# Performance work log

Hardware: AMD Instinct MI355X
Metric: run time of the kernel (lower is better)

The kernel has to match this reference:

```python
import jax, jax.numpy as jnp
import numpy as np

E = 1024
H = 16
HD = 64
DI = E // 16  # 64, GRU hidden size
VOCAB = 32000
B, T = 2, 2048


def adaptive_pool_matrix(l_in, l_out):
    # PyTorch AdaptiveAvgPool1d: out[i] = mean(in[floor(i*l_in/l_out) : ceil((i+1)*l_in/l_out)])
    P = np.zeros((l_in, l_out), np.float32)
    for i in range(l_out):
        s = (i * l_in) // l_out
        e = -((-(i + 1) * l_in) // l_out)
        P[s:e, i] = 1.0 / (e - s)
    return jnp.asarray(P)


def gru(x, wih, whh):
    # x: [B, T, DI]; wih/whh: [3*DI, DI]; no bias; gate order (r, z, n)
    h_dim = whh.shape[1]
    xw = jnp.einsum('btd,gd->btg', x, wih)  # [B, T, 3*DI]

    def step(h, xw_t):
        hw = h @ whh.T
        r = jax.nn.sigmoid(xw_t[:, :h_dim] + hw[:, :h_dim])
        z = jax.nn.sigmoid(xw_t[:, h_dim:2 * h_dim] + hw[:, h_dim:2 * h_dim])
        n = jnp.tanh(xw_t[:, 2 * h_dim:] + r * hw[:, 2 * h_dim:])
        h_new = (1.0 - z) * n + z * h
        return h_new, h_new

    h0 = jnp.zeros((x.shape[0], h_dim), x.dtype)
    _, hs = jax.lax.scan(step, h0, jnp.swapaxes(xw, 0, 1))
    return jnp.swapaxes(hs, 0, 1)  # [B, T, DI]


def pos_embed(x, gru_wih, gru_whh, lin_w, p_pos, p_proj):
    # x: [B, T, E]. Pools act on the feature dim (torch last-dim after permute).
    x_proj = x @ p_proj            # [B, T, E-DI]
    pos = gru(x @ p_pos, gru_wih, gru_whh)  # [B, T, DI]
    out = jnp.concatenate([pos, x_proj], axis=-1) @ lin_w.T
    return out + x


def layernorm(x, w, b, eps=1e-5):
    mu = jnp.mean(x, axis=-1, keepdims=True)
    var = jnp.var(x, axis=-1, keepdims=True)
    return (x - mu) * jax.lax.rsqrt(var + eps) * w + b


def setup_inputs() -> dict:
    key = jax.random.key(0)
    ks = jax.random.split(key, 16)
    s = 0.02
    return {
        'x': jax.random.normal(ks[0], (B, T, E), jnp.float32),
        'token_ids': jax.random.randint(ks[1], (B, T), 0, VOCAB, jnp.int32),
        'q_gru_wih': jax.random.normal(ks[2], (3 * DI, DI), jnp.float32) * s,
        'q_gru_whh': jax.random.normal(ks[3], (3 * DI, DI), jnp.float32) * s,
        'q_lin_w': jax.random.normal(ks[4], (E, E), jnp.float32) * s,
        'k_gru_wih': jax.random.normal(ks[5], (3 * DI, DI), jnp.float32) * s,
        'k_gru_whh': jax.random.normal(ks[6], (3 * DI, DI), jnp.float32) * s,
        'k_lin_w': jax.random.normal(ks[7], (E, E), jnp.float32) * s,
        'v_emb': jax.random.normal(ks[8], (VOCAB, E), jnp.float32) * s + 1.0,
        'q_ln_w': jnp.ones((E,), jnp.float32),
        'q_ln_b': jnp.zeros((E,), jnp.float32),
        'k_ln_w': jnp.ones((E,), jnp.float32),
        'k_ln_b': jnp.zeros((E,), jnp.float32),
        'out_w': jax.random.normal(ks[9], (E, E), jnp.float32) * s,
        'out_b': jnp.zeros((E,), jnp.float32),
    }


def reference(x, token_ids, q_gru_wih, q_gru_whh, q_lin_w, k_gru_wih, k_gru_whh,
              k_lin_w, v_emb, q_ln_w, q_ln_b, k_ln_w, k_ln_b, out_w, out_b):
    p_pos = adaptive_pool_matrix(E, DI)
    p_proj = adaptive_pool_matrix(E, E - DI)

    q = pos_embed(x, q_gru_wih, q_gru_whh, q_lin_w, p_pos, p_proj)
    k = pos_embed(x, k_gru_wih, k_gru_whh, k_lin_w, p_pos, p_proj)
    v = jax.nn.silu(x) * v_emb[token_ids]  # [B, T, E]

    q = layernorm(q, q_ln_w, q_ln_b)
    k = layernorm(k, k_ln_w, k_ln_b)

    # [B, T, E] -> [B, H, T, HD]
    def split_heads(t):
        return t.reshape(B, T, H, HD).transpose(0, 2, 1, 3)

    qh, kh, vh = split_heads(q), split_heads(k), split_heads(v)

    scores = jnp.einsum('bhtd,bhsd->bhts', qh, kh) / jnp.sqrt(jnp.float32(HD))
    # Original code: attn_weights += attn_weights.masked_fill(mask, -inf)
    # => unmasked scores are DOUBLED; masked (future) positions become -inf.
    causal = jnp.triu(jnp.ones((T, T), bool), k=1)  # True above diagonal
    scores = jnp.where(causal, -jnp.inf, scores * 2.0)
    attn = jax.nn.softmax(scores, axis=-1)

    out = jnp.einsum('bhts,bhsd->bhtd', attn, vh)  # [B, H, T, HD]
    out = out.transpose(0, 2, 1, 3).reshape(B, T, E)
    return out @ out_w.T + out_b
```

## Files before the change

kernel.cpp:

```cpp
#include <hip/hip_runtime.h>


namespace {

constexpr int B_ = 2, T_ = 2048, E_ = 1024, H_ = 16, HD_ = 64, G3_ = 192, M_ = B_ * T_;
constexpr float SRg = -1.4426950408889634f;
constexpr float SNg = 2.8853900817779268f;

typedef _Float16 f16;
typedef _Float16 f16x8 __attribute__((ext_vector_type(8)));
typedef _Float16 f16x4 __attribute__((ext_vector_type(4)));
typedef _Float16 f16x2 __attribute__((ext_vector_type(2)));
typedef float f32x4 __attribute__((ext_vector_type(4)));

__device__ __forceinline__ f32x4 mfma16(f16x8 a, f16x8 b, f32x4 c) {
  return __builtin_amdgcn_mfma_f32_16x16x32_f16(a, b, c, 0, 0, 0);
}

#if __has_builtin(__builtin_amdgcn_fdot2)
__device__ __forceinline__ float fdot2(f16x2 a, f16x2 b, float c) {
  return __builtin_amdgcn_fdot2(a, b, c, false);
}
#else
__device__ __forceinline__ float fdot2(f16x2 a, f16x2 b, float c) {
  return c + (float)a[0] * (float)b[0] + (float)a[1] * (float)b[1];
}
#endif

__device__ __forceinline__ float exp2_(float x) {
#if __has_builtin(__builtin_amdgcn_exp2f)
  return __builtin_amdgcn_exp2f(x);
#else
  return exp2f(x);
#endif
}
__device__ __forceinline__ float rcp_(float x) {
#if __has_builtin(__builtin_amdgcn_rcpf)
  return __builtin_amdgcn_rcpf(x);
#else
  return 1.f / x;
#endif
}

__global__ __launch_bounds__(256) void k_cvt(const float* __restrict__ s,
                                             f16* __restrict__ d, int n) {
  int i = (blockIdx.x * 256 + threadIdx.x) * 4;
  if (i < n) {
    float4 v = *(const float4*)(s + i);
    f16x4 o = {(f16)v.x, (f16)v.y, (f16)v.z, (f16)v.w};
    *(f16x4*)(d + i) = o;
  }
}

__global__ __launch_bounds__(256) void k_prep(
    const float* __restrict__ x, const int* __restrict__ tok,
    const f16* __restrict__ wihq, const f16* __restrict__ wihk,
    const float* __restrict__ v_emb,
    f16* __restrict__ vh, f16* __restrict__ aq, f16* __restrict__ ak,
    float* __restrict__ xwq, float* __restrict__ xwk) {
  __shared__ float xs[E_];
  __shared__ float xp[64];
  const int row = blockIdx.x;
  const int b = row >> 11, t = row & (T_ - 1);
  const int tid = threadIdx.x;
  const float* xrow = x + (size_t)row * E_;
  {
    const int tk = tok[row];
    float4 xv = ((const float4*)xrow)[tid];
    ((float4*)xs)[tid] = xv;
    float4 ev = ((const float4*)(v_emb + (size_t)tk * E_))[tid];
    f16x4 o;
    o[0] = (f16)(xv.x / (1.f + __expf(-xv.x)) * ev.x);
    o[1] = (f16)(xv.y / (1.f + __expf(-xv.y)) * ev.y);
    o[2] = (f16)(xv.z / (1.f + __expf(-xv.z)) * ev.z);
    o[3] = (f16)(xv.w / (1.f + __expf(-xv.w)) * ev.w);
    const int e0 = tid * 4;
    const size_t voff = ((size_t)(b * H_ + (e0 >> 6)) * T_ + t) * HD_ + (e0 & 63);
    *(f16x4*)(vh + voff) = o;
  }
  __syncthreads();
  if (tid < 64) {
    float s = 0.f;
#pragma unroll
    for (int j = 0; j < 16; ++j) s += xs[tid * 16 + j];
    xp[tid] = s * (1.f / 16.f);
  }
  for (int i = tid; i < 960; i += 256) {
    int s0 = (i * 1024) / 960;
    int e0 = ((i + 1) * 1024 + 959) / 960;
    float m = xs[s0];
    if (e0 - s0 == 2) m = (m + xs[s0 + 1]) * 0.5f;
    f16 hv = (f16)m;
    aq[(size_t)row * E_ + 64 + i] = hv;
    ak[(size_t)row * E_ + 64 + i] = hv;
  }
  __syncthreads();
  for (int o = tid; o < 2 * G3_; o += 256) {
    const int chain = o / G3_, g = o % G3_;
    const f16* wrow = (chain ? wihk : wihq) + g * 64;
    float acc = 0.f;
#pragma unroll
    for (int c = 0; c < 8; ++c) {
      f16x8 wv = *(const f16x8*)(wrow + c * 8);
#pragma unroll
      for (int u = 0; u < 8; ++u) acc += xp[c * 8 + u] * (float)wv[u];
    }
    const float sc = (g < 128) ? SRg : SNg;
    (chain ? xwk : xwq)[(size_t)row * G3_ + g] = acc * sc;
  }
}

__device__ __forceinline__ void gru_core(const float* __restrict__ xw,
                                         const float* __restrict__ whh,
                                         f16* __restrict__ a, int lane) {
  f16x2 wr[32], wz[32], wn[32];
#pragma unroll
  for (int i = 0; i < 32; ++i) {
    wr[i] = {(f16)(whh[(size_t)lane * 64 + i] * SRg),
             (f16)(whh[(size_t)lane * 64 + i + 32] * SRg)};
    wz[i] = {(f16)(whh[(size_t)(64 + lane) * 64 + i] * SRg),
             (f16)(whh[(size_t)(64 + lane) * 64 + i + 32] * SRg)};
    wn[i] = {(f16)(whh[(size_t)(128 + lane) * 64 + i] * SNg),
             (f16)(whh[(size_t)(128 + lane) * 64 + i + 32] * SNg)};
  }
  float h = 0.f;
  float xr = xw[lane], xz = xw[64 + lane], xn = xw[128 + lane];
  for (int t = 0; t < T_; ++t) {
    const unsigned hu = (unsigned)__builtin_bit_cast(unsigned short, (f16)h);
    int va = (int)hu, vb = (int)hu;
    asm volatile("v_permlane32_swap_b32 %0, %1" : "+v"(va), "+v"(vb));
    const int pk = (int)(hu | ((unsigned)va << 16));
    int hp[32];
#pragma unroll
    for (int i = 0; i < 32; ++i) hp[i] = __builtin_amdgcn_readlane(pk, i);
    const int tn = (t + 1 < T_) ? t + 1 : t;
    const float* nx = xw + (size_t)tn * G3_;
    const float nxr = nx[lane], nxz = nx[64 + lane], nxn = nx[128 + lane];
    float ar = xr;
#pragma unroll
    for (int i = 0; i < 32; ++i)
      ar = fdot2(wr[i], __builtin_bit_cast(f16x2, hp[i]), ar);
    const float r = rcp_(1.f + exp2_(ar));
    float an = 0.f;
#pragma unroll
    for (int i = 0; i < 32; ++i)
      an = fdot2(wn[i], __builtin_bit_cast(f16x2, hp[i]), an);
    const float p2 = fmaf(r, an, xn);
    const float n = fmaf(-2.f, rcp_(1.f + exp2_(p2)), 1.f);
    float az = xz;
#pragma unroll
    for (int i = 0; i < 32; ++i)
      az = fdot2(wz[i], __builtin_bit_cast(f16x2, hp[i]), az);
    const float z = rcp_(1.f + exp2_(az));
    h = fmaf(z, h - n, n);
    a[(size_t)t * E_ + lane] = (f16)h;
    xr = nxr; xz = nxz; xn = nxn;
  }
}

__global__ __launch_bounds__(256, 1) void k_mega(
    const float* __restrict__ xwq, const float* __restrict__ xwk,
    const float* __restrict__ whhq, const float* __restrict__ whhk,
    f16* __restrict__ aq, f16* __restrict__ ak,
    const f16* __restrict__ WQ, const f16* __restrict__ WK,
    float* __restrict__ QPRE, float* __restrict__ KPRE,
    const float* __restrict__ out_w, f16* __restrict__ WO) {
  __shared__ __align__(16) f16 As[128][72];
  __shared__ __align__(16) f16 Bs[128][72];
  const int bx = blockIdx.x;
  const int tid = threadIdx.x;
  if (bx == 0) {
    const int wid = tid >> 6, lane = tid & 63;
    const int qk = wid >> 1, b = wid & 1;
    const float* xw = (qk ? xwk : xwq) + (size_t)b * T_ * G3_;
    const float* whh = qk ? whhk : whhq;
    f16* a = (qk ? ak : aq) + (size_t)b * T_ * E_;
    gru_core(xw, whh, a, lane);
    return;
  }
  if (bx <= 512) {
    const int bid = bx - 1;
    const int chain = bid >> 8, tile = bid & 255;
    const int m0 = (tile >> 3) * 128, n0 = (tile & 7) * 128;
    const f16* A = chain ? ak : aq;
    const f16* W = chain ? WK : WQ;
    float* C = chain ? KPRE : QPRE;
    const int wid = tid >> 6, lane = tid & 63;
    const int wr = wid >> 1, wc = wid & 1;
    const int lg = lane >> 4, lc = lane & 15;
    f32x4 acc[4][4] = {};
    for (int kt = 64; kt < E_; kt += 64) {
#pragma unroll
      for (int it = 0; it < 4; ++it) {
        const int r = it * 32 + (tid >> 3);
        const int cs = (tid & 7) * 8;
        *(f16x8*)&As[r][cs] = *(const f16x8*)(A + (size_t)(m0 + r) * E_ + kt + cs);
        *(f16x8*)&Bs[r][cs] = *(const f16x8*)(W + (size_t)(n0 + r) * E_ + kt + cs);
      }
      __syncthreads();
      f16x8 af[4][2], bf[4][2];
#pragma unroll
      for (int mi = 0; mi < 4; ++mi)
#pragma unroll
        for (int ks = 0; ks < 2; ++ks) {
          af[mi][ks] = *(const f16x8*)&As[wr * 64 + mi * 16 + lc][ks * 32 + lg * 8];
          bf[mi][ks] = *(const f16x8*)&Bs[wc * 64 + mi * 16 + lc][ks * 32 + lg * 8];
        }
#pragma unroll
      for (int mi = 0; mi < 4; ++mi)
#pragma unroll
        for (int ni = 0; ni < 4; ++ni)
#pragma unroll
          for (int ks = 0; ks < 2; ++ks)
            acc[mi][ni] = mfma16(af[mi][ks], bf[ni][ks], acc[mi][ni]);
      __syncthreads();
    }
#pragma unroll
    for (int mi = 0; mi < 4; ++mi) {
      const int r0 = m0 + wr * 64 + mi * 16 + lg * 4;
#pragma unroll
      for (int ni = 0; ni < 4; ++ni) {
        const int col = n0 + wc * 64 + ni * 16 + lc;
#pragma unroll
        for (int q = 0; q < 4; ++q)
          C[(size_t)(r0 + q) * E_ + col] = acc[mi][ni][q];
      }
    }
    return;
  }
  {
    const int cb = bx - 513;
    for (int i = cb * 256 + tid; i < E_ * E_ / 4; i += 8 * 256) {
      float4 v = ((const float4*)out_w)[i];
      f16x4 o = {(f16)v.x, (f16)v.y, (f16)v.z, (f16)v.w};
      *(f16x4*)(WO + (size_t)i * 4) = o;
    }
  }
}

__global__ __launch_bounds__(256) void k_fix(
    const f16* __restrict__ aq, const f16* __restrict__ ak,
    const f16* __restrict__ WQ, const f16* __restrict__ WK,
    const float* __restrict__ x, float* __restrict__ QPRE,
    float* __restrict__ KPRE) {
  __shared__ __align__(16) f16 As[128][72];
  __shared__ __align__(16) f16 Bs[128][72];
  const int chain = blockIdx.z;
  const f16* A = chain ? ak : aq;
  const f16* W = chain ? WK : WQ;
  float* C = chain ? KPRE : QPRE;
  const int m0 = blockIdx.x * 128, n0 = blockIdx.y * 128;
  const int tid = threadIdx.x;
  const int wid = tid >> 6, lane = tid & 63;
  const int wr = wid >> 1, wc = wid & 1;
  const int lg = lane >> 4, lc = lane & 15;
#pragma unroll
  for (int it = 0; it < 4; ++it) {
    const int r = it * 32 + (tid >> 3);
    const int cs = (tid & 7) * 8;
    *(f16x8*)&As[r][cs] = *(const f16x8*)(A + (size_t)(m0 + r) * E_ + cs);
    *(f16x8*)&Bs[r][cs] = *(const f16x8*)(W + (size_t)(n0 + r) * E_ + cs);
  }
  __syncthreads();
  f32x4 acc[4][4] = {};
  f16x8 af[4][2], bf[4][2];
#pragma unroll
  for (int mi = 0; mi < 4; ++mi)
#pragma unroll
    for (int ks = 0; ks < 2; ++ks) {
      af[mi][ks] = *(const f16x8*)&As[wr * 64 + mi * 16 + lc][ks * 32 + lg * 8];
      bf[mi][ks] = *(const f16x8*)&Bs[wc * 64 + mi * 16 + lc][ks * 32 + lg * 8];
    }
#pragma unroll
  for (int mi = 0; mi < 4; ++mi)
#pragma unroll
    for (int ni = 0; ni < 4; ++ni)
#pragma unroll
      for (int ks = 0; ks < 2; ++ks)
        acc[mi][ni] = mfma16(af[mi][ks], bf[ni][ks], acc[mi][ni]);
#pragma unroll
  for (int mi = 0; mi < 4; ++mi) {
    const int r0 = m0 + wr * 64 + mi * 16 + lg * 4;
#pragma unroll
    for (int ni = 0; ni < 4; ++ni) {
      const int col = n0 + wc * 64 + ni * 16 + lc;
#pragma unroll
      for (int q = 0; q < 4; ++q) {
        const size_t idx = (size_t)(r0 + q) * E_ + col;
        C[idx] += acc[mi][ni][q] + x[idx];
      }
    }
  }
}

__global__ __launch_bounds__(256) void k_ln(
    const float* __restrict__ qpre, const float* __restrict__ kpre,
    const float* __restrict__ qw, const float* __restrict__ qb,
    const float* __restrict__ kw, const float* __restrict__ kb,
    f16* __restrict__ qh, f16* __restrict__ kh) {
  const int chain = blockIdx.y;
  const float* pre = chain ? kpre : qpre;
  const float* gw = chain ? kw : qw;
  const float* gb = chain ? kb : qb;
  f16* outp = chain ? kh : qh;
  const int row = blockIdx.x;
  const int tid = threadIdx.x;
  const float4 v = ((const float4*)(pre + (size_t)row * E_))[tid];
  float s = v.x + v.y + v.z + v.w;
  float s2 = v.x * v.x + v.y * v.y + v.z * v.z + v.w * v.w;
#pragma unroll
  for (int off = 32; off; off >>= 1) {
    s += __shfl_xor(s, off);
    s2 += __shfl_xor(s2, off);
  }
  __shared__ float red[8];
  const int wid = tid >> 6, lane = tid & 63;
  if (!lane) { red[wid] = s; red[4 + wid] = s2; }
  __syncthreads();
  s = red[0] + red[1] + red[2] + red[3];
  s2 = red[4] + red[5] + red[6] + red[7];
  const float mu = s * (1.f / E_);
  const float inv = rsqrtf(s2 * (1.f / E_) - mu * mu + 1e-5f);
  const float4 w4 = ((const float4*)gw)[tid];
  const float4 b4 = ((const float4*)gb)[tid];
  const int e0 = tid * 4;
  f16x4 o;
  o[0] = (f16)((v.x - mu) * inv * w4.x + b4.x);
  o[1] = (f16)((v.y - mu) * inv * w4.y + b4.y);
  o[2] = (f16)((v.z - mu) * inv * w4.z + b4.z);
  o[3] = (f16)((v.w - mu) * inv * w4.w + b4.w);
  const int b = row >> 11, t = row & (T_ - 1);
  const size_t off2 = ((size_t)(b * H_ + (e0 >> 6)) * T_ + t) * HD_ + (e0 & 63);
  *(f16x4*)(outp + off2) = o;
}

__global__ __launch_bounds__(256) void k_attn(const f16* __restrict__ Q,
                                              const f16* __restrict__ K,
                                              const f16* __restrict__ V,
                                              f16* __restrict__ AO) {
  __shared__ __align__(16) f16 Kt[64][72];
  __shared__ __align__(16) f16 Vt[64][72];
  __shared__ __align__(16) f16 Ps[4][16][72];
  const int qi = blockIdx.x, bh = blockIdx.y;
  const int b = bh >> 4, h = bh & 15;
  const int tid = threadIdx.x, wid = tid >> 6, lane = tid & 63;
  const int lg = lane >> 4, lc = lane & 15;
  const size_t hbase = (size_t)bh * T_ * HD_;
  const int qb = qi * 64;
  f16x8 qf[2];
  {
    const int qrow = qb + wid * 16 + lc;
#pragma unroll
    for (int ks = 0; ks < 2; ++ks)
      qf[ks] = *(const f16x8*)(Q + hbase + (size_t)qrow * HD_ + ks * 32 + lg * 8);
  }
  f32x4 o[4] = {};
  float m_run[4] = {-1e30f, -1e30f, -1e30f, -1e30f};
  float l_run[4] = {};
  const int qrow_d = qb + wid * 16 + lg * 4;
  for (int kt = 0; kt <= qi; ++kt) {
    {
      const int r = tid >> 2, cs = (tid & 3) * 16;
      const f16* ksrc = K + hbase + (size_t)(kt * 64 + r) * HD_ + cs;
      *(f16x8*)&Kt[r][cs] = *(const f16x8*)ksrc;
      *(f16x8*)&Kt[r][cs + 8] = *(const f16x8*)(ksrc + 8);
      const f16* vsrc = V + hbase + (size_t)(kt * 64 + lane) * HD_ + wid * 16;
      f16x8 va = *(const f16x8*)vsrc;
      f16x8 vb = *(const f16x8*)(vsrc + 8);
#pragma unroll
      for (int u = 0; u < 8; ++u) {
        Vt[wid * 16 + u][lane] = va[u];
        Vt[wid * 16 + 8 + u][lane] = vb[u];
      }
    }
    __syncthreads();
    f32x4 s[4] = {};
#pragma unroll
    for (int nt = 0; nt < 4; ++nt)
#pragma unroll
      for (int ks = 0; ks < 2; ++ks) {
        f16x8 kf = *(const f16x8*)&Kt[nt * 16 + lc][ks * 32 + lg * 8];
        s[nt] = mfma16(qf[ks], kf, s[nt]);
      }
    const bool diag = (kt == qi);
#pragma unroll
    for (int nt = 0; nt < 4; ++nt) {
      const int colg = kt * 64 + nt * 16 + lc;
#pragma unroll
      for (int r = 0; r < 4; ++r) {
        float v = s[nt][r] * 0.25f;
        if (diag && colg > qrow_d + r) v = -1e30f;
        s[nt][r] = v;
      }
    }
    float scalev[4];
#pragma unroll
    for (int r = 0; r < 4; ++r) {
      float m = fmaxf(fmaxf(s[0][r], s[1][r]), fmaxf(s[2][r], s[3][r]));
#pragma unroll
      for (int of = 1; of < 16; of <<= 1) m = fmaxf(m, __shfl_xor(m, of));
      const float mn = fmaxf(m_run[r], m);
      scalev[r] = __expf(m_run[r] - mn);
      m_run[r] = mn;
    }
    float ladd[4] = {};
#pragma unroll
    for (int nt = 0; nt < 4; ++nt)
#pragma unroll
      for (int r = 0; r < 4; ++r) {
        const float p = __expf(s[nt][r] - m_run[r]);
        s[nt][r] = p;
        ladd[r] += p;
      }
#pragma unroll
    for (int r = 0; r < 4; ++r) {
      float la = ladd[r];
#pragma unroll
      for (int of = 1; of < 16; of <<= 1) la += __shfl_xor(la, of);
      l_run[r] = l_run[r] * scalev[r] + la;
      o[0][r] *= scalev[r];
      o[1][r] *= scalev[r];
      o[2][r] *= scalev[r];
      o[3][r] *= scalev[r];
    }
#pragma unroll
    for (int nt = 0; nt < 4; ++nt)
#pragma unroll
      for (int r = 0; r < 4; ++r)
        Ps[wid][lg * 4 + r][nt * 16 + lc] = (f16)s[nt][r];
    f16x8 pf[2];
#pragma unroll
    for (int ks = 0; ks < 2; ++ks)
      pf[ks] = *(const f16x8*)&Ps[wid][lc][ks * 32 + lg * 8];
#pragma unroll
    for (int nt = 0; nt < 4; ++nt)
#pragma unroll
      for (int ks = 0; ks < 2; ++ks) {
        f16x8 vf = *(const f16x8*)&Vt[nt * 16 + lc][ks * 32 + lg * 8];
        o[nt] = mfma16(pf[ks], vf, o[nt]);
      }
    __syncthreads();
  }
#pragma unroll
  for (int nt = 0; nt < 4; ++nt)
#pragma unroll
    for (int r = 0; r < 4; ++r) {
      const float val = o[nt][r] / l_run[r];
      const int qrow = qrow_d + r;
      AO[((size_t)(b * T_ + qrow)) * E_ + h * HD_ + nt * 16 + lc] = (f16)val;
    }
}

__global__ __launch_bounds__(256) void k_gemm_out(
    const f16* __restrict__ A, const f16* __restrict__ W,
    const float* __restrict__ bias, float* __restrict__ C) {
  __shared__ __align__(16) f16 As[128][72];
  __shared__ __align__(16) f16 Bs[128][72];
  const int m0 = blockIdx.x * 128, n0 = blockIdx.y * 128;
  const int tid = threadIdx.x;
  const int wid = tid >> 6, lane = tid & 63;
  const int wr = wid >> 1, wc = wid & 1;
  const int lg = lane >> 4, lc = lane & 15;
  f32x4 acc[4][4] = {};
  for (int kt = 0; kt < E_; kt += 64) {
#pragma unroll
    for (int it = 0; it < 4; ++it) {
      const int r = it * 32 + (tid >> 3);
      const int cs = (tid & 7) * 8;
      *(f16x8*)&As[r][cs] = *(const f16x8*)(A + (size_t)(m0 + r) * E_ + kt + cs);
      *(f16x8*)&Bs[r][cs] = *(const f16x8*)(W + (size_t)(n0 + r) * E_ + kt + cs);
    }
    __syncthreads();
    f16x8 af[4][2], bf[4][2];
#pragma unroll
    for (int mi = 0; mi < 4; ++mi)
#pragma unroll
      for (int ks = 0; ks < 2; ++ks) {
        af[mi][ks] = *(const f16x8*)&As[wr * 64 + mi * 16 + lc][ks * 32 + lg * 8];
        bf[mi][ks] = *(const f16x8*)&Bs[wc * 64 + mi * 16 + lc][ks * 32 + lg * 8];
      }
#pragma unroll
    for (int mi = 0; mi < 4; ++mi)
#pragma unroll
      for (int ni = 0; ni < 4; ++ni)
#pragma unroll
        for (int ks = 0; ks < 2; ++ks)
          acc[mi][ni] = mfma16(af[mi][ks], bf[ni][ks], acc[mi][ni]);
    __syncthreads();
  }
#pragma unroll
  for (int mi = 0; mi < 4; ++mi) {
    const int r0 = m0 + wr * 64 + mi * 16 + lg * 4;
#pragma unroll
    for (int ni = 0; ni < 4; ++ni) {
      const int col = n0 + wc * 64 + ni * 16 + lc;
      const float bv = bias[col];
#pragma unroll
      for (int q = 0; q < 4; ++q)
        C[(size_t)(r0 + q) * E_ + col] = acc[mi][ni][q] + bv;
    }
  }
}

}

extern "C" void kernel_launch(void* const* d_in, const int* in_sizes, int n_in,
                              void* d_out, int out_size, void* d_ws, size_t ws_size,
                              hipStream_t stream) {
  (void)in_sizes; (void)n_in; (void)out_size; (void)ws_size;
  const float* x      = (const float*)d_in[0];
  const int*   tok    = (const int*)d_in[1];
  const float* q_wih  = (const float*)d_in[2];
  const float* q_whh  = (const float*)d_in[3];
  const float* q_lin  = (const float*)d_in[4];
  const float* k_wih  = (const float*)d_in[5];
  const float* k_whh  = (const float*)d_in[6];
  const float* k_lin  = (const float*)d_in[7];
  const float* v_emb  = (const float*)d_in[8];
  const float* q_ln_w = (const float*)d_in[9];
  const float* q_ln_b = (const float*)d_in[10];
  const float* k_ln_w = (const float*)d_in[11];
  const float* k_ln_b = (const float*)d_in[12];
  const float* out_w  = (const float*)d_in[13];
  const float* out_b  = (const float*)d_in[14];
  float* outp = (float*)d_out;

  char* ws = (char*)d_ws;
  size_t off = 0;
  auto take = [&](size_t bytes) -> void* {
    void* p = ws + off;
    off += (bytes + 255) & ~(size_t)255;
    return p;
  };
  f16* WQ   = (f16*)take((size_t)E_ * E_ * 2);
  f16* WK   = (f16*)take((size_t)E_ * E_ * 2);
  f16* WO   = (f16*)take((size_t)E_ * E_ * 2);
  f16* WIHQ = (f16*)take((size_t)G3_ * 64 * 2);
  f16* WIHK = (f16*)take((size_t)G3_ * 64 * 2);
  f16* AQ   = (f16*)take((size_t)M_ * E_ * 2);
  f16* AK   = (f16*)take((size_t)M_ * E_ * 2);
  f16* VH   = (f16*)take((size_t)M_ * E_ * 2);
  f16* QH   = (f16*)take((size_t)M_ * E_ * 2);
  f16* KH   = (f16*)take((size_t)M_ * E_ * 2);
  f16* AO   = (f16*)take((size_t)M_ * E_ * 2);
  float* XWQ  = (float*)take((size_t)M_ * G3_ * 4);
  float* XWK  = (float*)take((size_t)M_ * G3_ * 4);
  float* QPRE = (float*)take((size_t)M_ * E_ * 4);
  float* KPRE = (float*)take((size_t)M_ * E_ * 4);

  k_cvt<<<dim3((E_ * E_) / 1024), dim3(256), 0, stream>>>(q_lin, WQ, E_ * E_);
  k_cvt<<<dim3((E_ * E_) / 1024), dim3(256), 0, stream>>>(k_lin, WK, E_ * E_);
  k_cvt<<<dim3((G3_ * 64) / 1024), dim3(256), 0, stream>>>(q_wih, WIHQ, G3_ * 64);
  k_cvt<<<dim3((G3_ * 64) / 1024), dim3(256), 0, stream>>>(k_wih, WIHK, G3_ * 64);

  k_prep<<<dim3(M_), dim3(256), 0, stream>>>(x, tok, WIHQ, WIHK, v_emb, VH, AQ, AK, XWQ, XWK);

  k_mega<<<dim3(521), dim3(256), 0, stream>>>(XWQ, XWK, q_whh, k_whh, AQ, AK,
                                              WQ, WK, QPRE, KPRE, out_w, WO);

  k_fix<<<dim3(M_ / 128, E_ / 128, 2), dim3(256), 0, stream>>>(AQ, AK, WQ, WK, x, QPRE, KPRE);
  k_ln<<<dim3(M_, 2), dim3(256), 0, stream>>>(QPRE, KPRE, q_ln_w, q_ln_b, k_ln_w, k_ln_b, QH, KH);

  k_attn<<<dim3(T_ / 64, B_ * H_), dim3(256), 0, stream>>>(QH, KH, VH, AO);
  k_gemm_out<<<dim3(M_ / 128, E_ / 128), dim3(256), 0, stream>>>(AO, WO, out_b, outp);
}
```

Measured before the change: 883.6 us.

## Fuse weight fp16 conversion into GEMM staging and interleave GRU dot products

Removes the separate k_cvt launches by converting fp32 lin and wih weights to fp16 while staging them into shared memory inside the GEMM and prep kernels. The residual x add moves from k_fix into the k_mega epilogue. The GRU loop now runs its three gate dot products in one interleaved loop with readlanes done inline, and raises wave priority with s_setprio. The trade-off is that each GEMM tile rereads fp32 weights, doubling the weight bytes it loads, and the GRU's serial critical path may shift.

```diff
diff --git a/kernel.cpp b/kernel.cpp
--- a/kernel.cpp
+++ b/kernel.cpp
@@ -42,19 +42,25 @@
 #endif
 }
 
-__global__ __launch_bounds__(256) void k_cvt(const float* __restrict__ s,
-                                             f16* __restrict__ d, int n) {
-  int i = (blockIdx.x * 256 + threadIdx.x) * 4;
-  if (i < n) {
-    float4 v = *(const float4*)(s + i);
-    f16x4 o = {(f16)v.x, (f16)v.y, (f16)v.z, (f16)v.w};
-    *(f16x4*)(d + i) = o;
+__device__ __forceinline__ void stage_w_f32(const float* __restrict__ Wf,
+                                            f16 (*Bs)[72], int n0, int kt,
+                                            int tid) {
+#pragma unroll
+  for (int it = 0; it < 4; ++it) {
+    const int r = it * 32 + (tid >> 3);
+    const int cs = (tid & 7) * 8;
+    const float* src = Wf + (size_t)(n0 + r) * E_ + kt + cs;
+    float4 w0 = *(const float4*)src;
+    float4 w1 = *(const float4*)(src + 4);
+    f16x8 o = {(f16)w0.x, (f16)w0.y, (f16)w0.z, (f16)w0.w,
+               (f16)w1.x, (f16)w1.y, (f16)w1.z, (f16)w1.w};
+    *(f16x8*)&Bs[r][cs] = o;
   }
 }
 
 __global__ __launch_bounds__(256) void k_prep(
     const float* __restrict__ x, const int* __restrict__ tok,
-    const f16* __restrict__ wihq, const f16* __restrict__ wihk,
+    const float* __restrict__ wihq, const float* __restrict__ wihk,
     const float* __restrict__ v_emb,
     f16* __restrict__ vh, f16* __restrict__ aq, f16* __restrict__ ak,
     float* __restrict__ xwq, float* __restrict__ xwk) {
@@ -97,13 +103,13 @@
   __syncthreads();
   for (int o = tid; o < 2 * G3_; o += 256) {
     const int chain = o / G3_, g = o % G3_;
-    const f16* wrow = (chain ? wihk : wihq) + g * 64;
+    const float* wrow = (chain ? wihk : wihq) + (size_t)g * 64;
     float acc = 0.f;
 #pragma unroll
-    for (int c = 0; c < 8; ++c) {
-      f16x8 wv = *(const f16x8*)(wrow + c * 8);
-#pragma unroll
-      for (int u = 0; u < 8; ++u) acc += xp[c * 8 + u] * (float)wv[u];
+    for (int c = 0; c < 16; ++c) {
+      float4 wv = *(const float4*)(wrow + c * 4);
+      acc += xp[c * 4] * wv.x + xp[c * 4 + 1] * wv.y +
+             xp[c * 4 + 2] * wv.z + xp[c * 4 + 3] * wv.w;
     }
     const float sc = (g < 128) ? SRg : SNg;
     (chain ? xwk : xwq)[(size_t)row * G3_ + g] = acc * sc;
@@ -113,6 +119,7 @@
 __device__ __forceinline__ void gru_core(const float* __restrict__ xw,
                                          const float* __restrict__ whh,
                                          f16* __restrict__ a, int lane) {
+  __builtin_amdgcn_s_setprio(3);
   f16x2 wr[32], wz[32], wn[32];
 #pragma unroll
   for (int i = 0; i < 32; ++i) {
@@ -125,35 +132,29 @@
   }
   float h = 0.f;
   float xr = xw[lane], xz = xw[64 + lane], xn = xw[128 + lane];
+  f16* ap = a + lane;
   for (int t = 0; t < T_; ++t) {
     const unsigned hu = (unsigned)__builtin_bit_cast(unsigned short, (f16)h);
     int va = (int)hu, vb = (int)hu;
     asm volatile("v_permlane32_swap_b32 %0, %1" : "+v"(va), "+v"(vb));
     const int pk = (int)(hu | ((unsigned)va << 16));
-    int hp[32];
-#pragma unroll
-    for (int i = 0; i < 32; ++i) hp[i] = __builtin_amdgcn_readlane(pk, i);
     const int tn = (t + 1 < T_) ? t + 1 : t;
     const float* nx = xw + (size_t)tn * G3_;
     const float nxr = nx[lane], nxz = nx[64 + lane], nxn = nx[128 + lane];
-    float ar = xr;
-#pragma unroll
-    for (int i = 0; i < 32; ++i)
-      ar = fdot2(wr[i], __builtin_bit_cast(f16x2, hp[i]), ar);
+    float ar = xr, az = xz, an = 0.f;
+#pragma unroll
+    for (int i = 0; i < 32; ++i) {
+      const f16x2 hh = __builtin_bit_cast(f16x2, __builtin_amdgcn_readlane(pk, i));
+      ar = fdot2(wr[i], hh, ar);
+      an = fdot2(wn[i], hh, an);
+      az = fdot2(wz[i], hh, az);
+    }
     const float r = rcp_(1.f + exp2_(ar));
-    float an = 0.f;
-#pragma unroll
-    for (int i = 0; i < 32; ++i)
-      an = fdot2(wn[i], __builtin_bit_cast(f16x2, hp[i]), an);
     const float p2 = fmaf(r, an, xn);
     const float n = fmaf(-2.f, rcp_(1.f + exp2_(p2)), 1.f);
-    float az = xz;
-#pragma unroll
-    for (int i = 0; i < 32; ++i)
-      az = fdot2(wz[i], __builtin_bit_cast(f16x2, hp[i]), az);
     const float z = rcp_(1.f + exp2_(az));
     h = fmaf(z, h - n, n);
-    a[(size_t)t * E_ + lane] = (f16)h;
+    ap[(size_t)t * E_] = (f16)h;
     xr = nxr; xz = nxz; xn = nxn;
   }
 }
@@ -162,7 +163,8 @@
     const float* __restrict__ xwq, const float* __restrict__ xwk,
     const float* __restrict__ whhq, const float* __restrict__ whhk,
     f16* __restrict__ aq, f16* __restrict__ ak,
-    const f16* __restrict__ WQ, const f16* __restrict__ WK,
+    const float* __restrict__ WQf, const float* __restrict__ WKf,
+    const float* __restrict__ x,
     float* __restrict__ QPRE, float* __restrict__ KPRE,
     const float* __restrict__ out_w, f16* __restrict__ WO) {
   __shared__ __align__(16) f16 As[128][72];
@@ -183,7 +185,7 @@
     const int chain = bid >> 8, tile = bid & 255;
     const int m0 = (tile >> 3) * 128, n0 = (tile & 7) * 128;
     const f16* A = chain ? ak : aq;
-    const f16* W = chain ? WK : WQ;
+    const float* Wf = chain ? WKf : WQf;
     float* C = chain ? KPRE : QPRE;
     const int wid = tid >> 6, lane = tid & 63;
     const int wr = wid >> 1, wc = wid & 1;
@@ -195,8 +197,8 @@
         const int r = it * 32 + (tid >> 3);
         const int cs = (tid & 7) * 8;
         *(f16x8*)&As[r][cs] = *(const f16x8*)(A + (size_t)(m0 + r) * E_ + kt + cs);
-        *(f16x8*)&Bs[r][cs] = *(const f16x8*)(W + (size_t)(n0 + r) * E_ + kt + cs);
-      }
+      }
+      stage_w_f32(Wf, Bs, n0, kt, tid);
       __syncthreads();
       f16x8 af[4][2], bf[4][2];
 #pragma unroll
@@ -222,8 +224,10 @@
       for (int ni = 0; ni < 4; ++ni) {
         const int col = n0 + wc * 64 + ni * 16 + lc;
 #pragma unroll
-        for (int q = 0; q < 4; ++q)
-          C[(size_t)(r0 + q) * E_ + col] = acc[mi][ni][q];
+        for (int q = 0; q < 4; ++q) {
+          const size_t idx = (size_t)(r0 + q) * E_ + col;
+          C[idx] = acc[mi][ni][q] + x[idx];
+        }
       }
     }
     return;
@@ -240,14 +244,13 @@
 
 __global__ __launch_bounds__(256) void k_fix(
     const f16* __restrict__ aq, const f16* __restrict__ ak,
-    const f16* __restrict__ WQ, const f16* __restrict__ WK,
-    const float* __restrict__ x, float* __restrict__ QPRE,
-    float* __restrict__ KPRE) {
+    const float* __restrict__ WQf, const float* __restrict__ WKf,
+    float* __restrict__ QPRE, float* __restrict__ KPRE) {
   __shared__ __align__(16) f16 As[128][72];
   __shared__ __align__(16) f16 Bs[128][72];
   const int chain = blockIdx.z;
   const f16* A = chain ? ak : aq;
-  const f16* W = chain ? WK : WQ;
+  const float* Wf = chain ? WKf : WQf;
   float* C = chain ? KPRE : QPRE;
   const int m0 = blockIdx.x * 128, n0 = blockIdx.y * 128;
   const int tid = threadIdx.x;
@@ -259,8 +262,8 @@
     const int r = it * 32 + (tid >> 3);
     const int cs = (tid & 7) * 8;
     *(f16x8*)&As[r][cs] = *(const f16x8*)(A + (size_t)(m0 + r) * E_ + cs);
-    *(f16x8*)&Bs[r][cs] = *(const f16x8*)(W + (size_t)(n0 + r) * E_ + cs);
-  }
+  }
+  stage_w_f32(Wf, Bs, n0, 0, tid);
   __syncthreads();
   f32x4 acc[4][4] = {};
   f16x8 af[4][2], bf[4][2];
@@ -287,7 +290,7 @@
 #pragma unroll
       for (int q = 0; q < 4; ++q) {
         const size_t idx = (size_t)(r0 + q) * E_ + col;
-        C[idx] += acc[mi][ni][q] + x[idx];
+        C[idx] += acc[mi][ni][q];
       }
     }
   }
@@ -532,11 +535,7 @@
     off += (bytes + 255) & ~(size_t)255;
     return p;
   };
-  f16* WQ   = (f16*)take((size_t)E_ * E_ * 2);
-  f16* WK   = (f16*)take((size_t)E_ * E_ * 2);
   f16* WO   = (f16*)take((size_t)E_ * E_ * 2);
-  f16* WIHQ = (f16*)take((size_t)G3_ * 64 * 2);
-  f16* WIHK = (f16*)take((size_t)G3_ * 64 * 2);
   f16* AQ   = (f16*)take((size_t)M_ * E_ * 2);
   f16* AK   = (f16*)take((size_t)M_ * E_ * 2);
   f16* VH   = (f16*)take((size_t)M_ * E_ * 2);
@@ -548,17 +547,12 @@
   float* QPRE = (float*)take((size_t)M_ * E_ * 4);
   float* KPRE = (float*)take((size_t)M_ * E_ * 4);
 
-  k_cvt<<<dim3((E_ * E_) / 1024), dim3(256), 0, stream>>>(q_lin, WQ, E_ * E_);
-  k_cvt<<<dim3((E_ * E_) / 1024), dim3(256), 0, stream>>>(k_lin, WK, E_ * E_);
-  k_cvt<<<dim3((G3_ * 64) / 1024), dim3(256), 0, stream>>>(q_wih, WIHQ, G3_ * 64);
-  k_cvt<<<dim3((G3_ * 64) / 1024), dim3(256), 0, stream>>>(k_wih, WIHK, G3_ * 64);
-
-  k_prep<<<dim3(M_), dim3(256), 0, stream>>>(x, tok, WIHQ, WIHK, v_emb, VH, AQ, AK, XWQ, XWK);
+  k_prep<<<dim3(M_), dim3(256), 0, stream>>>(x, tok, q_wih, k_wih, v_emb, VH, AQ, AK, XWQ, XWK);
 
   k_mega<<<dim3(521), dim3(256), 0, stream>>>(XWQ, XWK, q_whh, k_whh, AQ, AK,
-                                              WQ, WK, QPRE, KPRE, out_w, WO);
-
-  k_fix<<<dim3(M_ / 128, E_ / 128, 2), dim3(256), 0, stream>>>(AQ, AK, WQ, WK, x, QPRE, KPRE);
+                                              q_lin, k_lin, x, QPRE, KPRE, out_w, WO);
+
+  k_fix<<<dim3(M_ / 128, E_ / 128, 2), dim3(256), 0, stream>>>(AQ, AK, q_lin, k_lin, QPRE, KPRE);
   k_ln<<<dim3(M_, 2), dim3(256), 0, stream>>>(QPRE, KPRE, q_ln_w, q_ln_b, k_ln_w, k_ln_b, QH, KH);
 
   k_attn<<<dim3(T_ / 64, B_ * H_), dim3(256), 0, stream>>>(QH, KH, VH, AO);
```

After: 879.9 us. No clear change (-0.4%).
